# Kernel tuning notes

Hardware: AMD Instinct MI355X
Metric: run time of the kernel (lower is better)

The kernel has to match this reference:

```python
import jax, jax.numpy as jnp
import numpy as np

# model dims
V, D, DFF, H, NL = 8192, 1024, 4096, 16, 4
B, L, M = 2, 2048, 2048
S, R, W = 64, 1, 512          # chunk_size, chunk_rank, window_len
DH = D // H
NC = (L + M) // S             # total chunks over klen
NMC = M // S                  # memory chunks
NQC = L // S                  # query chunks in current block
NCV = NC * R                  # number of compressed chunk vectors
NT = L // W                   # window tiles

# static index/mask helpers (host-side numpy)
TILE_IDX = np.arange(NT)[:, None] * W + np.arange(2 * W)[None, :]          # (NT,2W) overlapping key tiles
DIAG_IDX = np.arange(W)[:, None] + 1 + np.arange(W)[None, :]               # (W,W): query q attends tile keys q+1..q+W
CIDX = np.arange(2 * W)[None, :] - np.arange(W)[:, None] - 1               # inverse map tile col -> band col
CVALID = (CIDX >= 0) & (CIDX < W)
_dist = (NMC + np.arange(NQC))[:, None] - np.arange(NC)[None, :]           # chunk distance (query chunk - key chunk)
PIDX = np.clip((NC - 1 - _dist)[:, :, None] * R + np.arange(R)[None, None, :], 0, NCV - 1).reshape(NQC, NCV)
CMASK = np.repeat(np.triu(np.ones((NQC, NC), dtype=bool), k=NMC), R, axis=1)  # mask key chunks >= own chunk


def layer_norm(x, g, b, eps=1e-5):
    mu = jnp.mean(x, -1, keepdims=True)
    var = jnp.mean((x - mu) ** 2, -1, keepdims=True)
    return (x - mu) * jax.lax.rsqrt(var + eps) * g + b


def sin_pos_emb(pos_seq, d):
    inv = jnp.asarray(1.0 / (10000.0 ** (np.arange(0, d, 2) / float(d))), jnp.float32)
    ang = pos_seq[:, None] * inv[None, :]
    return jnp.concatenate([jnp.sin(ang), jnp.cos(ang)], axis=-1)


def ls_attention(h, cache, Wq, Wk, Wv, Wo, w_dc, b_dc, Wr, Wrc, brc, rw, rr, gd, bd, gw, bw, pos_win, key_pe):
    # h: (B,L,D), cache: (B,M,D)
    def compress(seq):  # dynamic low-rank chunk compression
        n_ch = seq.shape[1] // S
        sc = (seq @ w_dc + b_dc).reshape(B, n_ch, S, H, R)
        sc = jax.nn.softmax(sc, axis=2)                       # softmax over chunk positions
        v = seq.reshape(B, n_ch, S, H, DH)
        return jnp.einsum('bcshr,bcshd->bcrhd', sc, v).reshape(B, n_ch * R, D)

    comp = jnp.concatenate([compress(cache), compress(h)], axis=1)           # (B,NCV,D)
    kc = layer_norm(comp @ Wk, gd, bd).reshape(B, NCV, H, DH).transpose(0, 2, 1, 3)
    vc = layer_norm(comp @ Wv, gd, bd).reshape(B, NCV, H, DH).transpose(0, 2, 1, 3)

    hw = jnp.concatenate([cache[:, -W:], h], axis=1)                         # (B,W+L,D)
    kw = layer_norm(hw @ Wk, gw, bw).reshape(B, W + L, H, DH)
    vw = layer_norm(hw @ Wv, gw, bw).reshape(B, W + L, H, DH)

    q = (h @ Wq).reshape(B, L, H, DH).transpose(0, 2, 1, 3) / np.float32(np.sqrt(DH))
    qw = q + rw[None, :, None, :]   # content bias
    qr = q + rr[None, :, None, :]   # position bias

    # ---- sliding-window attention (band width W, via overlapping tiles) ----
    kt = kw[:, TILE_IDX]            # (B,NT,2W,H,DH)
    vt = vw[:, TILE_IDX]
    ts = jnp.einsum('bhtqd,btkhd->bhtqk', qw.reshape(B, H, NT, W, DH), kt)   # (B,H,NT,W,2W)
    band = jnp.take_along_axis(ts, jnp.asarray(DIAG_IDX)[None, None, None], axis=-1)  # (B,H,NT,W,W)
    Pw = (pos_win @ Wr).reshape(W, H, DH)
    win_scores = band.reshape(B, H, L, W) + jnp.einsum('bhld,whd->bhlw', qr, Pw)

    # ---- compressed chunk attention with chunk-level relative positions ----
    cs = jnp.einsum('bhld,bhcd->bhlc', qw, kc)                               # (B,H,L,NCV)
    Pc = (key_pe @ Wrc + brc).reshape(NCV, H, DH)
    raw = jnp.einsum('bhld,phd->bhlp', qr, Pc)
    aligned = jnp.take_along_axis(raw.reshape(B, H, NQC, S, NCV), jnp.asarray(PIDX)[None, None, :, None, :], axis=-1)
    ch = cs.reshape(B, H, NQC, S, NCV) + aligned
    ch = jnp.where(jnp.asarray(CMASK)[None, None, :, None, :], -1e30, ch).reshape(B, H, L, NCV)

    # joint softmax over [window keys | chunk summaries] (DualLN makes scales compatible)
    probs = jax.nn.softmax(jnp.concatenate([win_scores, ch], axis=-1), axis=-1)
    pw_, pc_ = probs[..., :W], probs[..., W:]

    gath = jnp.take_along_axis(pw_.reshape(B, H, NT, W, W), jnp.asarray(np.clip(CIDX, 0, W - 1))[None, None, None], axis=-1)
    tileP = jnp.where(jnp.asarray(CVALID)[None, None, None], gath, 0.0)      # (B,H,NT,W,2W)
    out_w = jnp.einsum('bhtqk,btkhd->bhtqd', tileP, vt).reshape(B, H, L, DH)
    out_c = jnp.einsum('bhlc,bhcd->bhld', pc_, vc)
    return (out_w + out_c).transpose(0, 2, 1, 3).reshape(B, L, D) @ Wo


def setup_inputs() -> dict:
    key = jax.random.key(0)
    ks = jax.random.split(key, 20)
    n = lambda i, shape, s=0.02: jax.random.normal(ks[i], shape, jnp.float32) * s
    z = lambda shape: jnp.zeros(shape, jnp.float32)
    return {
        'x': jax.random.randint(ks[0], (B, L), 0, V, dtype=jnp.int32),
        'cache': n(1, (NL, B, M, D), 0.1),
        'emb': n(2, (V, D), float(D) ** -0.5),
        'out_bias': z((V,)),
        'Wq': n(3, (NL, D, D)), 'Wk': n(4, (NL, D, D)), 'Wv': n(5, (NL, D, D)), 'Wo': n(6, (NL, D, D)),
        'w_dc': n(7, (NL, D, H * R)), 'b_dc': z((NL, H * R)),
        'Wr': n(8, (NL, D, D)), 'Wrc': n(9, (NL, D, D)), 'brc': z((NL, D)),
        'rw': n(10, (NL, H, DH)), 'rr': n(11, (NL, H, DH)),
        'g1': 1.0 + n(12, (NL, D)), 'b1': z((NL, D)),
        'g2': 1.0 + n(13, (NL, D)), 'b2': z((NL, D)),
        'gd': 1.0 + n(14, (NL, D)), 'bd': z((NL, D)),
        'gw': 1.0 + n(15, (NL, D)), 'bw': z((NL, D)),
        'wf1': n(16, (NL, D, DFF)), 'bf1': z((NL, DFF)),
        'wf2': n(17, (NL, DFF, D)), 'bf2': z((NL, D)),
    }


def reference(x, cache, emb, out_bias, Wq, Wk, Wv, Wo, w_dc, b_dc, Wr, Wrc, brc, rw, rr,
              g1, b1, g2, b2, gd, bd, gw, bw, wf1, bf1, wf2, bf2):
    h = emb[x] * np.float32(np.sqrt(D))
    pos_win = sin_pos_emb(jnp.arange(W - 1, -1, -1, dtype=jnp.float32), D)
    key_pe = sin_pos_emb(jnp.arange(NCV - 1, -1, -1, dtype=jnp.float32), D)
    for l in range(NL):  # post-LN (pre_ln=False)
        a = ls_attention(h, cache[l], Wq[l], Wk[l], Wv[l], Wo[l], w_dc[l], b_dc[l], Wr[l], Wrc[l],
                         brc[l], rw[l], rr[l], gd[l], bd[l], gw[l], bw[l], pos_win, key_pe)
        h = layer_norm(h + a, g1[l], b1[l])
        ff = jax.nn.gelu(h @ wf1[l] + bf1[l], approximate=False) @ wf2[l] + bf2[l]
        h = layer_norm(h + ff, g2[l], b2[l])
    logits = h @ emb.T + out_bias   # tied output embedding
    return jax.nn.log_softmax(logits, axis=-1)
```

## Files before the change

kernel.cpp:

```cpp
#include <hip/hip_runtime.h>
#include <math.h>

constexpr int Bq   = 2;
constexpr int Lq   = 2048;
constexpr int Mq   = 2048;
constexpr int Dq   = 1024;
constexpr int DFFq = 4096;
constexpr int Hq   = 16;
constexpr int DHq  = 64;
constexpr int Vq   = 8192;
constexpr int NLq  = 4;
constexpr int Wwin = 512;
constexpr int NCVq = 64;
constexpr int HWLEN = Wwin + Lq;

constexpr size_t OFF_H    = 0;
constexpr size_t OFF_A    = OFF_H    + (size_t)Bq*Lq*Dq;
constexpr size_t OFF_ATT  = OFF_A    + (size_t)Bq*Lq*Dq;
constexpr size_t OFF_Q    = OFF_ATT  + (size_t)Bq*Lq*Dq;
constexpr size_t OFF_HW   = OFF_Q    + (size_t)Bq*Lq*Dq;
constexpr size_t OFF_KW   = OFF_HW   + (size_t)Bq*HWLEN*Dq;
constexpr size_t OFF_VW   = OFF_KW   + (size_t)Bq*HWLEN*Dq;
constexpr size_t OFF_FF   = OFF_VW   + (size_t)Bq*HWLEN*Dq;
constexpr size_t OFF_COMP = OFF_FF   + (size_t)Bq*Lq*DFFq;
constexpr size_t OFF_KC   = OFF_COMP + (size_t)Bq*NCVq*Dq;
constexpr size_t OFF_VC   = OFF_KC   + (size_t)Bq*NCVq*Dq;
constexpr size_t OFF_SCC  = OFF_VC   + (size_t)Bq*NCVq*Dq;
constexpr size_t OFF_SCH  = OFF_SCC  + (size_t)Bq*Mq*16;
constexpr size_t OFF_PWIN = OFF_SCH  + (size_t)Bq*Lq*16;
constexpr size_t OFF_KPE  = OFF_PWIN + (size_t)Wwin*Dq;
constexpr size_t OFF_PW   = OFF_KPE  + (size_t)NCVq*Dq;
constexpr size_t OFF_PC   = OFF_PW   + (size_t)Wwin*Dq;
constexpr size_t WS_FLOATS= OFF_PC   + (size_t)NCVq*Dq;

__global__ __launch_bounds__(256) void embed_kernel(const int* __restrict__ x,
                                                    const float* __restrict__ emb,
                                                    float* __restrict__ h) {
  int i = blockIdx.x * 256 + threadIdx.x;
  int tok = i >> 10;
  int d = i & 1023;
  h[i] = emb[(size_t)x[tok] * Dq + d] * 32.0f;
}

__global__ __launch_bounds__(256) void posemb_kernel(float* __restrict__ pwin,
                                                     float* __restrict__ kpe) {
  int i = blockIdx.x * 256 + threadIdx.x;
  int row = i >> 10, col = i & 1023;
  int ii = col & 511;
  bool is_cos = col >= 512;
  float invf = (float)exp(-((double)(2 * ii) / 1024.0) * log(10000.0));
  float* dst; float pos;
  if (row < Wwin) { dst = pwin + (size_t)row * Dq + col; pos = (float)(Wwin - 1 - row); }
  else { dst = kpe + (size_t)(row - Wwin) * Dq + col; pos = (float)(NCVq - 1 - (row - Wwin)); }
  float ang = pos * invf;
  *dst = is_cos ? cosf(ang) : sinf(ang);
}

template<int BT, int EPI>
__global__ __launch_bounds__(256) void gemm_kernel(const float* __restrict__ A,
                                                   const float* __restrict__ Bm,
                                                   const float* __restrict__ bias,
                                                   float* __restrict__ C,
                                                   int M, int N, int K) {
  __shared__ float As[16][64];
  __shared__ float Bs[16][64];
  const int tid = threadIdx.x;
  const int tx = tid & 15;
  const int ty = tid >> 4;
  const int m0 = blockIdx.y * 64;
  const int n0 = blockIdx.x * 64;
  const int ar = tid >> 2;
  const int ak = (tid & 3) << 2;
  float acc[4][4] = {};
  for (int k0 = 0; k0 < K; k0 += 16) {
    float4 av = *(const float4*)(A + (size_t)(m0 + ar) * K + (k0 + ak));
    As[ak + 0][ar] = av.x; As[ak + 1][ar] = av.y;
    As[ak + 2][ar] = av.z; As[ak + 3][ar] = av.w;
    if (BT == 0) {
      const int bk = tid >> 4;
      const int bc = (tid & 15) << 2;
      float4 bv = make_float4(0.f, 0.f, 0.f, 0.f);
      if (n0 + bc < N) bv = *(const float4*)(Bm + (size_t)(k0 + bk) * N + (n0 + bc));
      Bs[bk][bc + 0] = bv.x; Bs[bk][bc + 1] = bv.y;
      Bs[bk][bc + 2] = bv.z; Bs[bk][bc + 3] = bv.w;
    } else {
      const int c = tid >> 2;
      const int kk = (tid & 3) << 2;
      float4 bv = make_float4(0.f, 0.f, 0.f, 0.f);
      if (n0 + c < N) bv = *(const float4*)(Bm + (size_t)(n0 + c) * K + (k0 + kk));
      Bs[kk + 0][c] = bv.x; Bs[kk + 1][c] = bv.y;
      Bs[kk + 2][c] = bv.z; Bs[kk + 3][c] = bv.w;
    }
    __syncthreads();
#pragma unroll
    for (int k = 0; k < 16; ++k) {
      float4 a4 = *(const float4*)&As[k][ty << 2];
      float4 b4 = *(const float4*)&Bs[k][tx << 2];
      float aa[4] = {a4.x, a4.y, a4.z, a4.w};
      float bb[4] = {b4.x, b4.y, b4.z, b4.w};
#pragma unroll
      for (int i = 0; i < 4; ++i)
#pragma unroll
        for (int j = 0; j < 4; ++j) acc[i][j] += aa[i] * bb[j];
    }
    __syncthreads();
  }
  const int cbase = n0 + (tx << 2);
  if (cbase < N) {
#pragma unroll
    for (int i = 0; i < 4; ++i) {
      const int r = m0 + (ty << 2) + i;
      float4 o;
      float* op = &o.x;
#pragma unroll
      for (int j = 0; j < 4; ++j) {
        float v = acc[i][j];
        if (EPI >= 1) v += bias[cbase + j];
        if (EPI == 2) v = 0.5f * v * (1.0f + erff(v * 0.70710678118654752f));
        op[j] = v;
      }
      *(float4*)(C + (size_t)r * N + cbase) = o;
    }
  }
}

__global__ __launch_bounds__(256) void ln_kernel(const float* __restrict__ x,
                                                 const float* __restrict__ res,
                                                 const float* __restrict__ g,
                                                 const float* __restrict__ b,
                                                 float* __restrict__ out) {
  __shared__ float sm[4];
  const int row = blockIdx.x;
  const int t = threadIdx.x;
  const float* xp = x + (size_t)row * Dq;
  float v[4];
#pragma unroll
  for (int i = 0; i < 4; ++i) v[i] = xp[t + 256 * i];
  if (res) {
    const float* rp = res + (size_t)row * Dq;
#pragma unroll
    for (int i = 0; i < 4; ++i) v[i] += rp[t + 256 * i];
  }
  float s = v[0] + v[1] + v[2] + v[3];
#pragma unroll
  for (int off = 32; off > 0; off >>= 1) s += __shfl_down(s, off);
  if ((t & 63) == 0) sm[t >> 6] = s;
  __syncthreads();
  const float mu = (sm[0] + sm[1] + sm[2] + sm[3]) * (1.0f / Dq);
  __syncthreads();
  float s2 = 0.f;
#pragma unroll
  for (int i = 0; i < 4; ++i) { float d = v[i] - mu; s2 += d * d; }
#pragma unroll
  for (int off = 32; off > 0; off >>= 1) s2 += __shfl_down(s2, off);
  if ((t & 63) == 0) sm[t >> 6] = s2;
  __syncthreads();
  const float var = (sm[0] + sm[1] + sm[2] + sm[3]) * (1.0f / Dq);
  const float rstd = rsqrtf(var + 1e-5f);
  float* op = out + (size_t)row * Dq;
#pragma unroll
  for (int i = 0; i < 4; ++i) {
    int c = t + 256 * i;
    op[c] = (v[i] - mu) * rstd * g[c] + b[c];
  }
}

__global__ __launch_bounds__(64) void compress_kernel(const float* __restrict__ scc,
                                                      const float* __restrict__ sch,
                                                      const float* __restrict__ cache_l,
                                                      const float* __restrict__ h,
                                                      float* __restrict__ comp) {
  const int bi = blockIdx.x;
  const int head = bi & 15;
  const int c = (bi >> 4) & 63;
  const int b = bi >> 10;
  const bool from_cache = c < 32;
  const int cc = from_cache ? c : c - 32;
  const float* logits = (from_cache ? scc : sch) + (size_t)(b * 2048 + cc * 64) * 16 + head;
  const float* seq = (from_cache ? cache_l : h) + (size_t)(b * 2048 + cc * 64) * Dq + head * 64;
  __shared__ float wsm[64];
  const int t = threadIdx.x;
  wsm[t] = logits[(size_t)t * 16];
  __syncthreads();
  float mx = -1e30f;
#pragma unroll 8
  for (int s = 0; s < 64; ++s) mx = fmaxf(mx, wsm[s]);
  float sum = 0.f;
#pragma unroll 8
  for (int s = 0; s < 64; ++s) sum += expf(wsm[s] - mx);
  float myw = expf(wsm[t] - mx) / sum;
  __syncthreads();
  wsm[t] = myw;
  __syncthreads();
  float acc = 0.f;
#pragma unroll 4
  for (int s = 0; s < 64; ++s) acc += wsm[s] * seq[(size_t)s * Dq + t];
  comp[(size_t)(b * 64 + c) * Dq + head * 64 + t] = acc;
}

__global__ __launch_bounds__(256) void hwbuild_kernel(const float* __restrict__ cache_l,
                                                      const float* __restrict__ h,
                                                      float* __restrict__ hw) {
  int i = blockIdx.x * 256 + threadIdx.x;
  const int D4 = Dq / 4;
  int d4 = i % D4;
  int r = (i / D4) % HWLEN;
  int b = i / (HWLEN * D4);
  const float4* src;
  if (r < Wwin) src = (const float4*)(cache_l + (size_t)(b * Mq + (Mq - Wwin) + r) * Dq) + d4;
  else          src = (const float4*)(h + (size_t)(b * Lq + (r - Wwin)) * Dq) + d4;
  ((float4*)hw)[i] = *src;
}

__global__ __launch_bounds__(256) void attn_kernel(const float* __restrict__ q,
                                                   const float* __restrict__ kw,
                                                   const float* __restrict__ vw,
                                                   const float* __restrict__ kc,
                                                   const float* __restrict__ vc,
                                                   const float* __restrict__ Pw,
                                                   const float* __restrict__ Pc,
                                                   const float* __restrict__ rw,
                                                   const float* __restrict__ rr,
                                                   float* __restrict__ att) {
  __shared__ float qws[32][64];
  __shared__ float qrs[32][64];
  __shared__ float sc[32][580];
  __shared__ float ksf[64 * 64];
  const int blk = blockIdx.x;
  const int qblk = blk & 63;
  const int hh = (blk >> 6) & 15;
  const int b = blk >> 10;
  const int qbase = qblk * 32;
  const int qc = qblk >> 1;
  const int t = threadIdx.x;
  const int hoff = hh * 64;

#pragma unroll
  for (int i = 0; i < 8; ++i) {
    int e = t + 256 * i;
    int qi = e >> 6, d = e & 63;
    float qv = q[(size_t)(b * Lq + qbase + qi) * Dq + hoff + d] * 0.125f;
    qws[qi][d] = qv + rw[hoff + d];
    qrs[qi][d] = qv + rr[hoff + d];
  }
  __syncthreads();

  const int eq = t >> 6;
  const int ed = t & 63;

  for (int cb = 0; cb < 8; ++cb) {
#pragma unroll
    for (int i = 0; i < 16; ++i) {
      int e = t + 256 * i;
      int jj = e >> 6, d = e & 63;
      ksf[jj * 64 + (d ^ ((jj & 7) << 2))] = Pw[(size_t)(cb * 64 + jj) * Dq + hoff + d];
    }
    __syncthreads();
#pragma unroll
    for (int rs = 0; rs < 8; ++rs) {
      int qi = eq + 4 * rs;
      int jj = ed;
      float dot = 0.f;
#pragma unroll
      for (int d0 = 0; d0 < 64; d0 += 4) {
        float4 qv = *(const float4*)&qrs[qi][d0];
        float4 kv = *(const float4*)&ksf[jj * 64 + (d0 ^ ((jj & 7) << 2))];
        dot += qv.x * kv.x + qv.y * kv.y + qv.z * kv.z + qv.w * kv.w;
      }
      sc[qi][cb * 64 + jj] = dot;
    }
    __syncthreads();
  }

  for (int ci = 0; ci < 9; ++ci) {
    const int khw0 = qbase + 1 + ci * 64;
#pragma unroll
    for (int i = 0; i < 16; ++i) {
      int e = t + 256 * i;
      int kk = e >> 6, d = e & 63;
      int khw = khw0 + kk; if (khw > HWLEN - 1) khw = HWLEN - 1;
      ksf[kk * 64 + (d ^ ((kk & 7) << 2))] = kw[(size_t)(b * HWLEN + khw) * Dq + hoff + d];
    }
    __syncthreads();
#pragma unroll
    for (int rs = 0; rs < 8; ++rs) {
      int qi = eq + 4 * rs;
      int kk = ed;
      int j = ci * 64 + kk - qi;
      if (j >= 0 && j < 512) {
        float dot = 0.f;
#pragma unroll
        for (int d0 = 0; d0 < 64; d0 += 4) {
          float4 qv = *(const float4*)&qws[qi][d0];
          float4 kv = *(const float4*)&ksf[kk * 64 + (d0 ^ ((kk & 7) << 2))];
          dot += qv.x * kv.x + qv.y * kv.y + qv.z * kv.z + qv.w * kv.w;
        }
        sc[qi][j] += dot;
      }
    }
    __syncthreads();
  }

#pragma unroll
  for (int i = 0; i < 16; ++i) {
    int e = t + 256 * i;
    int cc = e >> 6, d = e & 63;
    ksf[cc * 64 + (d ^ ((cc & 7) << 2))] = kc[(size_t)(b * 64 + cc) * Dq + hoff + d];
  }
  __syncthreads();
#pragma unroll
  for (int rs = 0; rs < 8; ++rs) {
    int qi = eq + 4 * rs;
    int cc = ed;
    float dot = 0.f;
#pragma unroll
    for (int d0 = 0; d0 < 64; d0 += 4) {
      float4 qv = *(const float4*)&qws[qi][d0];
      float4 kv = *(const float4*)&ksf[cc * 64 + (d0 ^ ((cc & 7) << 2))];
      dot += qv.x * kv.x + qv.y * kv.y + qv.z * kv.z + qv.w * kv.w;
    }
    sc[qi][512 + cc] = dot;
  }
  __syncthreads();
#pragma unroll
  for (int i = 0; i < 16; ++i) {
    int e = t + 256 * i;
    int cc = e >> 6, d = e & 63;
    int pidx = 31 - qc + cc;
    pidx = pidx < 0 ? 0 : (pidx > 63 ? 63 : pidx);
    ksf[cc * 64 + (d ^ ((cc & 7) << 2))] = Pc[(size_t)pidx * Dq + hoff + d];
  }
  __syncthreads();
#pragma unroll
  for (int rs = 0; rs < 8; ++rs) {
    int qi = eq + 4 * rs;
    int cc = ed;
    float dot = 0.f;
#pragma unroll
    for (int d0 = 0; d0 < 64; d0 += 4) {
      float4 qv = *(const float4*)&qrs[qi][d0];
      float4 kv = *(const float4*)&ksf[cc * 64 + (d0 ^ ((cc & 7) << 2))];
      dot += qv.x * kv.x + qv.y * kv.y + qv.z * kv.z + qv.w * kv.w;
    }
    float vvv = sc[qi][512 + cc] + dot;
    sc[qi][512 + cc] = (cc >= qc + 32) ? -1e30f : vvv;
  }
  __syncthreads();

  {
    const int row = t >> 3;
    const int sub = t & 7;
    float m = -1e30f;
    for (int k = 0; k < 72; ++k) m = fmaxf(m, sc[row][sub + 8 * k]);
#pragma unroll
    for (int off = 1; off < 8; off <<= 1) m = fmaxf(m, __shfl_xor(m, off, 8));
    float ssum = 0.f;
    for (int k = 0; k < 72; ++k) ssum += expf(sc[row][sub + 8 * k] - m);
#pragma unroll
    for (int off = 1; off < 8; off <<= 1) ssum += __shfl_xor(ssum, off, 8);
    const float inv = 1.0f / ssum;
    for (int k = 0; k < 72; ++k) {
      int idx = sub + 8 * k;
      sc[row][idx] = expf(sc[row][idx] - m) * inv;
    }
  }
  __syncthreads();

  float acc[8] = {};
  const size_t vwbase = (size_t)b * HWLEN * Dq + hoff + ed;
  for (int j = 0; j < 512; ++j) {
#pragma unroll
    for (int rs = 0; rs < 8; ++rs) {
      int qi = eq + 4 * rs;
      acc[rs] += sc[qi][j] * vw[vwbase + (size_t)(qbase + qi + 1 + j) * Dq];
    }
  }
  const size_t vcbase = (size_t)b * 64 * Dq + hoff + ed;
  for (int cc = 0; cc < 64; ++cc) {
#pragma unroll
    for (int rs = 0; rs < 8; ++rs) {
      int qi = eq + 4 * rs;
      acc[rs] += sc[qi][512 + cc] * vc[vcbase + (size_t)cc * Dq];
    }
  }
#pragma unroll
  for (int rs = 0; rs < 8; ++rs) {
    int qi = eq + 4 * rs;
    att[(size_t)(b * Lq + qbase + qi) * Dq + hoff + ed] = acc[rs];
  }
}

__global__ __launch_bounds__(256) void logsoftmax_kernel(float* __restrict__ out) {
  __shared__ float sm[4];
  const int row = blockIdx.x;
  float* p = out + (size_t)row * Vq;
  const int t = threadIdx.x;
  float v[32];
  float m = -1e30f;
#pragma unroll
  for (int i = 0; i < 32; ++i) { v[i] = p[t + 256 * i]; m = fmaxf(m, v[i]); }
#pragma unroll
  for (int off = 32; off > 0; off >>= 1) m = fmaxf(m, __shfl_xor(m, off));
  if ((t & 63) == 0) sm[t >> 6] = m;
  __syncthreads();
  m = fmaxf(fmaxf(sm[0], sm[1]), fmaxf(sm[2], sm[3]));
  __syncthreads();
  float s = 0.f;
#pragma unroll
  for (int i = 0; i < 32; ++i) s += expf(v[i] - m);
#pragma unroll
  for (int off = 32; off > 0; off >>= 1) s += __shfl_down(s, off);
  if ((t & 63) == 0) sm[t >> 6] = s;
  __syncthreads();
  const float lse = m + logf(sm[0] + sm[1] + sm[2] + sm[3]);
#pragma unroll
  for (int i = 0; i < 32; ++i) p[t + 256 * i] = v[i] - lse;
}

extern "C" void kernel_launch(void* const* d_in, const int* in_sizes, int n_in,
                              void* d_out, int out_size, void* d_ws, size_t ws_size,
                              hipStream_t stream) {
  if (ws_size < WS_FLOATS * sizeof(float)) return;

  const int*   x        = (const int*)d_in[0];
  const float* cache    = (const float*)d_in[1];
  const float* emb      = (const float*)d_in[2];
  const float* out_bias = (const float*)d_in[3];
  const float* Wqw      = (const float*)d_in[4];
  const float* Wkw      = (const float*)d_in[5];
  const float* Wvw      = (const float*)d_in[6];
  const float* Wow      = (const float*)d_in[7];
  const float* w_dc     = (const float*)d_in[8];
  const float* b_dc     = (const float*)d_in[9];
  const float* Wr       = (const float*)d_in[10];
  const float* Wrc      = (const float*)d_in[11];
  const float* brc      = (const float*)d_in[12];
  const float* rw       = (const float*)d_in[13];
  const float* rr       = (const float*)d_in[14];
  const float* g1       = (const float*)d_in[15];
  const float* b1       = (const float*)d_in[16];
  const float* g2       = (const float*)d_in[17];
  const float* b2       = (const float*)d_in[18];
  const float* gd       = (const float*)d_in[19];
  const float* bd       = (const float*)d_in[20];
  const float* gw       = (const float*)d_in[21];
  const float* bw       = (const float*)d_in[22];
  const float* wf1      = (const float*)d_in[23];
  const float* bf1      = (const float*)d_in[24];
  const float* wf2      = (const float*)d_in[25];
  const float* bf2      = (const float*)d_in[26];

  float* ws   = (float*)d_ws;
  float* hbuf = ws + OFF_H;
  float* abuf = ws + OFF_A;
  float* attb = ws + OFF_ATT;
  float* qb   = ws + OFF_Q;
  float* hwb  = ws + OFF_HW;
  float* kwb  = ws + OFF_KW;
  float* vwb  = ws + OFF_VW;
  float* ffb  = ws + OFF_FF;
  float* comp = ws + OFF_COMP;
  float* kcb  = ws + OFF_KC;
  float* vcb  = ws + OFF_VC;
  float* scc  = ws + OFF_SCC;
  float* sch  = ws + OFF_SCH;
  float* pwin = ws + OFF_PWIN;
  float* kpe  = ws + OFF_KPE;
  float* Pwb  = ws + OFF_PW;
  float* Pcb  = ws + OFF_PC;
  float* outp = (float*)d_out;

  embed_kernel<<<(Bq * Lq * Dq) / 256, 256, 0, stream>>>(x, emb, hbuf);
  posemb_kernel<<<((Wwin + NCVq) * Dq) / 256, 256, 0, stream>>>(pwin, kpe);

  for (int l = 0; l < NLq; ++l) {
    const float* cache_l = cache + (size_t)l * Bq * Mq * Dq;
    const float* Wq_l  = Wqw + (size_t)l * Dq * Dq;
    const float* Wk_l  = Wkw + (size_t)l * Dq * Dq;
    const float* Wv_l  = Wvw + (size_t)l * Dq * Dq;
    const float* Wo_l  = Wow + (size_t)l * Dq * Dq;
    const float* wdc_l = w_dc + (size_t)l * Dq * 16;
    const float* bdc_l = b_dc + (size_t)l * 16;
    const float* Wr_l  = Wr  + (size_t)l * Dq * Dq;
    const float* Wrc_l = Wrc + (size_t)l * Dq * Dq;
    const float* brc_l = brc + (size_t)l * Dq;
    const float* rw_l  = rw  + (size_t)l * Hq * DHq;
    const float* rr_l  = rr  + (size_t)l * Hq * DHq;
    const float* g1_l  = g1 + (size_t)l * Dq;  const float* b1_l = b1 + (size_t)l * Dq;
    const float* g2_l  = g2 + (size_t)l * Dq;  const float* b2_l = b2 + (size_t)l * Dq;
    const float* gd_l  = gd + (size_t)l * Dq;  const float* bd_l = bd + (size_t)l * Dq;
    const float* gw_l  = gw + (size_t)l * Dq;  const float* bw_l = bw + (size_t)l * Dq;
    const float* wf1_l = wf1 + (size_t)l * Dq * DFFq;
    const float* bf1_l = bf1 + (size_t)l * DFFq;
    const float* wf2_l = wf2 + (size_t)l * DFFq * Dq;
    const float* bf2_l = bf2 + (size_t)l * Dq;

    gemm_kernel<0, 1><<<dim3(1, 64), 256, 0, stream>>>(cache_l, wdc_l, bdc_l, scc, Bq * Mq, 16, Dq);
    gemm_kernel<0, 1><<<dim3(1, 64), 256, 0, stream>>>(hbuf, wdc_l, bdc_l, sch, Bq * Lq, 16, Dq);
    compress_kernel<<<Bq * 64 * Hq, 64, 0, stream>>>(scc, sch, cache_l, hbuf, comp);
    gemm_kernel<0, 0><<<dim3(16, 2), 256, 0, stream>>>(comp, Wk_l, nullptr, kcb, Bq * NCVq, Dq, Dq);
    ln_kernel<<<Bq * NCVq, 256, 0, stream>>>(kcb, nullptr, gd_l, bd_l, kcb);
    gemm_kernel<0, 0><<<dim3(16, 2), 256, 0, stream>>>(comp, Wv_l, nullptr, vcb, Bq * NCVq, Dq, Dq);
    ln_kernel<<<Bq * NCVq, 256, 0, stream>>>(vcb, nullptr, gd_l, bd_l, vcb);
    hwbuild_kernel<<<(Bq * HWLEN * (Dq / 4)) / 256, 256, 0, stream>>>(cache_l, hbuf, hwb);
    gemm_kernel<0, 0><<<dim3(16, 80), 256, 0, stream>>>(hwb, Wk_l, nullptr, kwb, Bq * HWLEN, Dq, Dq);
    ln_kernel<<<Bq * HWLEN, 256, 0, stream>>>(kwb, nullptr, gw_l, bw_l, kwb);
    gemm_kernel<0, 0><<<dim3(16, 80), 256, 0, stream>>>(hwb, Wv_l, nullptr, vwb, Bq * HWLEN, Dq, Dq);
    ln_kernel<<<Bq * HWLEN, 256, 0, stream>>>(vwb, nullptr, gw_l, bw_l, vwb);
    gemm_kernel<0, 0><<<dim3(16, 64), 256, 0, stream>>>(hbuf, Wq_l, nullptr, qb, Bq * Lq, Dq, Dq);
    gemm_kernel<0, 0><<<dim3(16, 8), 256, 0, stream>>>(pwin, Wr_l, nullptr, Pwb, Wwin, Dq, Dq);
    gemm_kernel<0, 1><<<dim3(16, 1), 256, 0, stream>>>(kpe, Wrc_l, brc_l, Pcb, NCVq, Dq, Dq);
    attn_kernel<<<Bq * Hq * 64, 256, 0, stream>>>(qb, kwb, vwb, kcb, vcb, Pwb, Pcb, rw_l, rr_l, attb);
    gemm_kernel<0, 0><<<dim3(16, 64), 256, 0, stream>>>(attb, Wo_l, nullptr, abuf, Bq * Lq, Dq, Dq);
    ln_kernel<<<Bq * Lq, 256, 0, stream>>>(hbuf, abuf, g1_l, b1_l, hbuf);
    gemm_kernel<0, 2><<<dim3(64, 64), 256, 0, stream>>>(hbuf, wf1_l, bf1_l, ffb, Bq * Lq, DFFq, Dq);
    gemm_kernel<0, 1><<<dim3(16, 64), 256, 0, stream>>>(ffb, wf2_l, bf2_l, abuf, Bq * Lq, Dq, DFFq);
    ln_kernel<<<Bq * Lq, 256, 0, stream>>>(hbuf, abuf, g2_l, b2_l, hbuf);
  }

  gemm_kernel<1, 1><<<dim3(Vq / 64, (Bq * Lq) / 64), 256, 0, stream>>>(hbuf, emb, out_bias, outp,
                                                                       Bq * Lq, Vq, Dq);
  logsoftmax_kernel<<<Bq * Lq, 256, 0, stream>>>(outp);
}
```

Measured before the change: 16.99 ms.

## Move large GEMMs to bf16 MFMA kernels and restructure attention for 1024 threads

Replaces the fp32 SIMT GEMMs for the projection, FFN and output-logit matmuls with a bf16 MFMA GEMM using global_load_lds staging. Weights are transposed and converted to bf16 every call, and activations are converted before each GEMM. The attention kernel is reworked to use 1024 threads, and its PV stage now stages V tiles through LDS instead of reading global memory per element. The conversion kernels add traffic, and bf16 inputs lower precision compared with fp32.

```diff
diff --git a/kernel.cpp b/kernel.cpp
--- a/kernel.cpp
+++ b/kernel.cpp
@@ -7,31 +7,56 @@
 constexpr int Dq   = 1024;
 constexpr int DFFq = 4096;
 constexpr int Hq   = 16;
-constexpr int DHq  = 64;
 constexpr int Vq   = 8192;
 constexpr int NLq  = 4;
 constexpr int Wwin = 512;
 constexpr int NCVq = 64;
 constexpr int HWLEN = Wwin + Lq;
 
-constexpr size_t OFF_H    = 0;
-constexpr size_t OFF_A    = OFF_H    + (size_t)Bq*Lq*Dq;
-constexpr size_t OFF_ATT  = OFF_A    + (size_t)Bq*Lq*Dq;
-constexpr size_t OFF_Q    = OFF_ATT  + (size_t)Bq*Lq*Dq;
-constexpr size_t OFF_HW   = OFF_Q    + (size_t)Bq*Lq*Dq;
-constexpr size_t OFF_KW   = OFF_HW   + (size_t)Bq*HWLEN*Dq;
-constexpr size_t OFF_VW   = OFF_KW   + (size_t)Bq*HWLEN*Dq;
-constexpr size_t OFF_FF   = OFF_VW   + (size_t)Bq*HWLEN*Dq;
-constexpr size_t OFF_COMP = OFF_FF   + (size_t)Bq*Lq*DFFq;
-constexpr size_t OFF_KC   = OFF_COMP + (size_t)Bq*NCVq*Dq;
-constexpr size_t OFF_VC   = OFF_KC   + (size_t)Bq*NCVq*Dq;
-constexpr size_t OFF_SCC  = OFF_VC   + (size_t)Bq*NCVq*Dq;
-constexpr size_t OFF_SCH  = OFF_SCC  + (size_t)Bq*Mq*16;
-constexpr size_t OFF_PWIN = OFF_SCH  + (size_t)Bq*Lq*16;
-constexpr size_t OFF_KPE  = OFF_PWIN + (size_t)Wwin*Dq;
-constexpr size_t OFF_PW   = OFF_KPE  + (size_t)NCVq*Dq;
-constexpr size_t OFF_PC   = OFF_PW   + (size_t)Wwin*Dq;
-constexpr size_t WS_FLOATS= OFF_PC   + (size_t)NCVq*Dq;
+constexpr size_t F_H    = 0;
+constexpr size_t F_ATT  = F_H    + 4194304;
+constexpr size_t F_Q    = F_ATT  + 4194304;
+constexpr size_t F_HW   = F_Q    + 4194304;
+constexpr size_t F_KW   = F_HW   + 5242880;
+constexpr size_t F_VW   = F_KW   + 5242880;
+constexpr size_t F_COMP = F_VW   + 5242880;
+constexpr size_t F_KC   = F_COMP + 131072;
+constexpr size_t F_VC   = F_KC   + 131072;
+constexpr size_t F_SCC  = F_VC   + 131072;
+constexpr size_t F_SCH  = F_SCC  + 65536;
+constexpr size_t F_PWIN = F_SCH  + 65536;
+constexpr size_t F_KPE  = F_PWIN + 524288;
+constexpr size_t F_PWB  = F_KPE  + 65536;
+constexpr size_t F_PCB  = F_PWB  + 524288;
+constexpr size_t F_BF   = F_PCB  + 65536;
+constexpr size_t U_WT     = 0;
+constexpr size_t U_WQT    = U_WT + 0;
+constexpr size_t U_WKT    = U_WT + 1048576;
+constexpr size_t U_WVT    = U_WT + 2097152;
+constexpr size_t U_WOT    = U_WT + 3145728;
+constexpr size_t U_WRT    = U_WT + 4194304;
+constexpr size_t U_WF1T   = U_WT + 5242880;
+constexpr size_t U_WF2T   = U_WT + 9437184;
+constexpr size_t U_HBF    = 13631488;
+constexpr size_t U_HWBF   = U_HBF + 4194304;
+constexpr size_t U_FFBF   = U_HWBF + 5242880;
+constexpr size_t U_COMPBF = U_FFBF + 16777216;
+constexpr size_t U_PWINBF = U_COMPBF + 131072;
+constexpr size_t U_END    = U_PWINBF + 524288;
+constexpr size_t WS_FLOATS = F_BF + (U_END + 1) / 2;
+
+__device__ __forceinline__ unsigned short f2bf(float f) {
+  union { float f; unsigned u; } c; c.f = f;
+  unsigned u = c.u + 0x7fffu + ((c.u >> 16) & 1u);
+  return (unsigned short)(u >> 16);
+}
+
+typedef __attribute__((ext_vector_type(8))) short short8v;
+typedef __attribute__((ext_vector_type(4))) float f32x4v;
+
+#define GLOAD16(gp, lp)                                                              \
+  __builtin_amdgcn_global_load_lds((const __attribute__((address_space(1))) void*)(gp), \
+                                   (__attribute__((address_space(3))) void*)(lp), 16, 0, 0)
 
 __global__ __launch_bounds__(256) void embed_kernel(const int* __restrict__ x,
                                                     const float* __restrict__ emb,
@@ -54,6 +79,108 @@
   else { dst = kpe + (size_t)(row - Wwin) * Dq + col; pos = (float)(NCVq - 1 - (row - Wwin)); }
   float ang = pos * invf;
   *dst = is_cos ? cosf(ang) : sinf(ang);
+}
+
+__global__ __launch_bounds__(256) void cvt_bf16_kernel(const float* __restrict__ in,
+                                                       unsigned short* __restrict__ out) {
+  int i = blockIdx.x * 256 + threadIdx.x;
+  float4 v = ((const float4*)in)[i];
+  ushort4 o;
+  o.x = f2bf(v.x); o.y = f2bf(v.y); o.z = f2bf(v.z); o.w = f2bf(v.w);
+  ((ushort4*)out)[i] = o;
+}
+
+__global__ __launch_bounds__(256) void tcvt_kernel(const float* __restrict__ W,
+                                                   unsigned short* __restrict__ Wt,
+                                                   int K, int N) {
+  __shared__ float tile[64][65];
+  const int n0 = blockIdx.x * 64, k0 = blockIdx.y * 64;
+  const int tr = threadIdx.x >> 6;
+  const int tc = threadIdx.x & 63;
+#pragma unroll
+  for (int i = 0; i < 16; ++i) {
+    int r = i * 4 + tr;
+    tile[r][tc] = W[(size_t)(k0 + r) * N + n0 + tc];
+  }
+  __syncthreads();
+#pragma unroll
+  for (int i = 0; i < 16; ++i) {
+    int r = i * 4 + tr;
+    Wt[(size_t)(n0 + r) * K + k0 + tc] = f2bf(tile[tc][r]);
+  }
+}
+
+template<int EPI>
+__global__ __launch_bounds__(256) void gemm_bf16_kernel(const unsigned short* __restrict__ A,
+                                                        const unsigned short* __restrict__ Bt,
+                                                        const float* __restrict__ bias,
+                                                        void* __restrict__ Cout,
+                                                        int M, int N, int K) {
+  __shared__ unsigned short ldsA[8 * 512];
+  __shared__ unsigned short ldsB[8 * 512];
+  const int t = threadIdx.x;
+  const int wave = t >> 6, lane = t & 63;
+  const int m0 = blockIdx.y * 128, n0 = blockIdx.x * 128;
+  const int fr = lane & 15, fg = lane >> 4;
+  const unsigned short* Ab = A + (size_t)(m0 + fr) * K + fg * 8;
+  const unsigned short* Bb = Bt + (size_t)(n0 + fr) * K + fg * 8;
+  const int wr = wave >> 1, wc = wave & 1;
+  f32x4v acc[4][4];
+#pragma unroll
+  for (int i = 0; i < 4; ++i)
+#pragma unroll
+    for (int j = 0; j < 4; ++j) acc[i][j] = (f32x4v){0.f, 0.f, 0.f, 0.f};
+
+  for (int k0 = 0; k0 < K; k0 += 32) {
+    __syncthreads();
+    if (wave < 2) {
+#pragma unroll
+      for (int i = 0; i < 4; ++i) {
+        int sb = wave * 4 + i;
+        GLOAD16(Ab + (size_t)(sb * 16) * K + k0, &ldsA[sb * 512]);
+      }
+    } else {
+#pragma unroll
+      for (int i = 0; i < 4; ++i) {
+        int sb = (wave - 2) * 4 + i;
+        GLOAD16(Bb + (size_t)(sb * 16) * K + k0, &ldsB[sb * 512]);
+      }
+    }
+    __syncthreads();
+    short8v af[4], bf[4];
+#pragma unroll
+    for (int i = 0; i < 4; ++i) {
+      af[i] = *(const short8v*)&ldsA[(wr * 4 + i) * 512 + lane * 8];
+      bf[i] = *(const short8v*)&ldsB[(wc * 4 + i) * 512 + lane * 8];
+    }
+#pragma unroll
+    for (int i = 0; i < 4; ++i)
+#pragma unroll
+      for (int j = 0; j < 4; ++j)
+        acc[i][j] = __builtin_amdgcn_mfma_f32_16x16x32_bf16(af[i], bf[j], acc[i][j], 0, 0, 0);
+  }
+
+  const int orow0 = m0 + wr * 64 + (lane >> 4) * 4;
+  const int ocol0 = n0 + wc * 64 + (lane & 15);
+#pragma unroll
+  for (int i = 0; i < 4; ++i) {
+#pragma unroll
+    for (int j = 0; j < 4; ++j) {
+      const int col = ocol0 + j * 16;
+      float bv = (EPI >= 1) ? bias[col] : 0.f;
+#pragma unroll
+      for (int r = 0; r < 4; ++r) {
+        const int row = orow0 + i * 16 + r;
+        float v = acc[i][j][r] + bv;
+        if (EPI == 2) {
+          v = 0.5f * v * (1.0f + erff(v * 0.70710678118654752f));
+          ((unsigned short*)Cout)[(size_t)row * N + col] = f2bf(v);
+        } else {
+          ((float*)Cout)[(size_t)row * N + col] = v;
+        }
+      }
+    }
+  }
 }
 
 template<int BT, int EPI>
@@ -212,20 +339,20 @@
   ((float4*)hw)[i] = *src;
 }
 
-__global__ __launch_bounds__(256) void attn_kernel(const float* __restrict__ q,
-                                                   const float* __restrict__ kw,
-                                                   const float* __restrict__ vw,
-                                                   const float* __restrict__ kc,
-                                                   const float* __restrict__ vc,
-                                                   const float* __restrict__ Pw,
-                                                   const float* __restrict__ Pc,
-                                                   const float* __restrict__ rw,
-                                                   const float* __restrict__ rr,
-                                                   float* __restrict__ att) {
+__global__ __launch_bounds__(1024) void attn_kernel(const float* __restrict__ q,
+                                                    const float* __restrict__ kw,
+                                                    const float* __restrict__ vw,
+                                                    const float* __restrict__ kc,
+                                                    const float* __restrict__ vc,
+                                                    const float* __restrict__ Pw,
+                                                    const float* __restrict__ Pc,
+                                                    const float* __restrict__ rw,
+                                                    const float* __restrict__ rr,
+                                                    float* __restrict__ att) {
   __shared__ float qws[32][64];
   __shared__ float qrs[32][64];
   __shared__ float sc[32][580];
-  __shared__ float ksf[64 * 64];
+  __shared__ float ksf[4096];
   const int blk = blockIdx.x;
   const int qblk = blk & 63;
   const int hh = (blk >> 6) & 15;
@@ -236,8 +363,8 @@
   const int hoff = hh * 64;
 
 #pragma unroll
-  for (int i = 0; i < 8; ++i) {
-    int e = t + 256 * i;
+  for (int i = 0; i < 2; ++i) {
+    int e = t + 1024 * i;
     int qi = e >> 6, d = e & 63;
     float qv = q[(size_t)(b * Lq + qbase + qi) * Dq + hoff + d] * 0.125f;
     qws[qi][d] = qv + rw[hoff + d];
@@ -250,24 +377,23 @@
 
   for (int cb = 0; cb < 8; ++cb) {
 #pragma unroll
-    for (int i = 0; i < 16; ++i) {
-      int e = t + 256 * i;
+    for (int i = 0; i < 4; ++i) {
+      int e = t + 1024 * i;
       int jj = e >> 6, d = e & 63;
       ksf[jj * 64 + (d ^ ((jj & 7) << 2))] = Pw[(size_t)(cb * 64 + jj) * Dq + hoff + d];
     }
     __syncthreads();
 #pragma unroll
-    for (int rs = 0; rs < 8; ++rs) {
-      int qi = eq + 4 * rs;
-      int jj = ed;
+    for (int rs = 0; rs < 2; ++rs) {
+      int qi = eq + 16 * rs;
       float dot = 0.f;
 #pragma unroll
       for (int d0 = 0; d0 < 64; d0 += 4) {
         float4 qv = *(const float4*)&qrs[qi][d0];
-        float4 kv = *(const float4*)&ksf[jj * 64 + (d0 ^ ((jj & 7) << 2))];
+        float4 kv = *(const float4*)&ksf[ed * 64 + (d0 ^ ((ed & 7) << 2))];
         dot += qv.x * kv.x + qv.y * kv.y + qv.z * kv.z + qv.w * kv.w;
       }
-      sc[qi][cb * 64 + jj] = dot;
+      sc[qi][cb * 64 + ed] = dot;
     }
     __syncthreads();
   }
@@ -275,24 +401,23 @@
   for (int ci = 0; ci < 9; ++ci) {
     const int khw0 = qbase + 1 + ci * 64;
 #pragma unroll
-    for (int i = 0; i < 16; ++i) {
-      int e = t + 256 * i;
+    for (int i = 0; i < 4; ++i) {
+      int e = t + 1024 * i;
       int kk = e >> 6, d = e & 63;
       int khw = khw0 + kk; if (khw > HWLEN - 1) khw = HWLEN - 1;
       ksf[kk * 64 + (d ^ ((kk & 7) << 2))] = kw[(size_t)(b * HWLEN + khw) * Dq + hoff + d];
     }
     __syncthreads();
 #pragma unroll
-    for (int rs = 0; rs < 8; ++rs) {
-      int qi = eq + 4 * rs;
-      int kk = ed;
-      int j = ci * 64 + kk - qi;
+    for (int rs = 0; rs < 2; ++rs) {
+      int qi = eq + 16 * rs;
+      int j = ci * 64 + ed - qi;
       if (j >= 0 && j < 512) {
         float dot = 0.f;
 #pragma unroll
         for (int d0 = 0; d0 < 64; d0 += 4) {
           float4 qv = *(const float4*)&qws[qi][d0];
-          float4 kv = *(const float4*)&ksf[kk * 64 + (d0 ^ ((kk & 7) << 2))];
+          float4 kv = *(const float4*)&ksf[ed * 64 + (d0 ^ ((ed & 7) << 2))];
           dot += qv.x * kv.x + qv.y * kv.y + qv.z * kv.z + qv.w * kv.w;
         }
         sc[qi][j] += dot;
@@ -301,93 +426,121 @@
     __syncthreads();
   }
 
-#pragma unroll
-  for (int i = 0; i < 16; ++i) {
-    int e = t + 256 * i;
-    int cc = e >> 6, d = e & 63;
-    ksf[cc * 64 + (d ^ ((cc & 7) << 2))] = kc[(size_t)(b * 64 + cc) * Dq + hoff + d];
-  }
-  __syncthreads();
-#pragma unroll
-  for (int rs = 0; rs < 8; ++rs) {
-    int qi = eq + 4 * rs;
-    int cc = ed;
-    float dot = 0.f;
-#pragma unroll
-    for (int d0 = 0; d0 < 64; d0 += 4) {
-      float4 qv = *(const float4*)&qws[qi][d0];
-      float4 kv = *(const float4*)&ksf[cc * 64 + (d0 ^ ((cc & 7) << 2))];
-      dot += qv.x * kv.x + qv.y * kv.y + qv.z * kv.z + qv.w * kv.w;
-    }
-    sc[qi][512 + cc] = dot;
-  }
-  __syncthreads();
-#pragma unroll
-  for (int i = 0; i < 16; ++i) {
-    int e = t + 256 * i;
-    int cc = e >> 6, d = e & 63;
-    int pidx = 31 - qc + cc;
-    pidx = pidx < 0 ? 0 : (pidx > 63 ? 63 : pidx);
-    ksf[cc * 64 + (d ^ ((cc & 7) << 2))] = Pc[(size_t)pidx * Dq + hoff + d];
-  }
-  __syncthreads();
-#pragma unroll
-  for (int rs = 0; rs < 8; ++rs) {
-    int qi = eq + 4 * rs;
-    int cc = ed;
-    float dot = 0.f;
-#pragma unroll
-    for (int d0 = 0; d0 < 64; d0 += 4) {
-      float4 qv = *(const float4*)&qrs[qi][d0];
-      float4 kv = *(const float4*)&ksf[cc * 64 + (d0 ^ ((cc & 7) << 2))];
-      dot += qv.x * kv.x + qv.y * kv.y + qv.z * kv.z + qv.w * kv.w;
-    }
-    float vvv = sc[qi][512 + cc] + dot;
-    sc[qi][512 + cc] = (cc >= qc + 32) ? -1e30f : vvv;
-  }
-  __syncthreads();
-
   {
-    const int row = t >> 3;
-    const int sub = t & 7;
+#pragma unroll
+    for (int i = 0; i < 4; ++i) {
+      int e = t + 1024 * i;
+      int cc = e >> 6, d = e & 63;
+      ksf[cc * 64 + (d ^ ((cc & 7) << 2))] = kc[(size_t)(b * 64 + cc) * Dq + hoff + d];
+    }
+    __syncthreads();
+#pragma unroll
+    for (int rs = 0; rs < 2; ++rs) {
+      int qi = eq + 16 * rs;
+      float dot = 0.f;
+#pragma unroll
+      for (int d0 = 0; d0 < 64; d0 += 4) {
+        float4 qv = *(const float4*)&qws[qi][d0];
+        float4 kv = *(const float4*)&ksf[ed * 64 + (d0 ^ ((ed & 7) << 2))];
+        dot += qv.x * kv.x + qv.y * kv.y + qv.z * kv.z + qv.w * kv.w;
+      }
+      sc[qi][512 + ed] = dot;
+    }
+    __syncthreads();
+  }
+  {
+#pragma unroll
+    for (int i = 0; i < 4; ++i) {
+      int e = t + 1024 * i;
+      int cc = e >> 6, d = e & 63;
+      int pidx = 31 - qc + cc;
+      pidx = pidx < 0 ? 0 : (pidx > 63 ? 63 : pidx);
+      ksf[cc * 64 + (d ^ ((cc & 7) << 2))] = Pc[(size_t)pidx * Dq + hoff + d];
+    }
+    __syncthreads();
+#pragma unroll
+    for (int rs = 0; rs < 2; ++rs) {
+      int qi = eq + 16 * rs;
+      float dot = 0.f;
+#pragma unroll
+      for (int d0 = 0; d0 < 64; d0 += 4) {
+        float4 qv = *(const float4*)&qrs[qi][d0];
+        float4 kv = *(const float4*)&ksf[ed * 64 + (d0 ^ ((ed & 7) << 2))];
+        dot += qv.x * kv.x + qv.y * kv.y + qv.z * kv.z + qv.w * kv.w;
+      }
+      float vvv = sc[qi][512 + ed] + dot;
+      sc[qi][512 + ed] = (ed >= qc + 32) ? -1e30f : vvv;
+    }
+    __syncthreads();
+  }
+
+  {
+    const int row = t >> 5;
+    const int sub = t & 31;
     float m = -1e30f;
-    for (int k = 0; k < 72; ++k) m = fmaxf(m, sc[row][sub + 8 * k]);
-#pragma unroll
-    for (int off = 1; off < 8; off <<= 1) m = fmaxf(m, __shfl_xor(m, off, 8));
+#pragma unroll
+    for (int k = 0; k < 18; ++k) m = fmaxf(m, sc[row][sub + 32 * k]);
+#pragma unroll
+    for (int off = 1; off < 32; off <<= 1) m = fmaxf(m, __shfl_xor(m, off, 32));
     float ssum = 0.f;
-    for (int k = 0; k < 72; ++k) ssum += expf(sc[row][sub + 8 * k] - m);
-#pragma unroll
-    for (int off = 1; off < 8; off <<= 1) ssum += __shfl_xor(ssum, off, 8);
+#pragma unroll
+    for (int k = 0; k < 18; ++k) {
+      float p = expf(sc[row][sub + 32 * k] - m);
+      sc[row][sub + 32 * k] = p;
+      ssum += p;
+    }
+#pragma unroll
+    for (int off = 1; off < 32; off <<= 1) ssum += __shfl_xor(ssum, off, 32);
     const float inv = 1.0f / ssum;
-    for (int k = 0; k < 72; ++k) {
-      int idx = sub + 8 * k;
-      sc[row][idx] = expf(sc[row][idx] - m) * inv;
-    }
-  }
-  __syncthreads();
-
-  float acc[8] = {};
-  const size_t vwbase = (size_t)b * HWLEN * Dq + hoff + ed;
-  for (int j = 0; j < 512; ++j) {
-#pragma unroll
-    for (int rs = 0; rs < 8; ++rs) {
-      int qi = eq + 4 * rs;
-      acc[rs] += sc[qi][j] * vw[vwbase + (size_t)(qbase + qi + 1 + j) * Dq];
-    }
-  }
-  const size_t vcbase = (size_t)b * 64 * Dq + hoff + ed;
-  for (int cc = 0; cc < 64; ++cc) {
-#pragma unroll
-    for (int rs = 0; rs < 8; ++rs) {
-      int qi = eq + 4 * rs;
-      acc[rs] += sc[qi][512 + cc] * vc[vcbase + (size_t)cc * Dq];
-    }
-  }
-#pragma unroll
-  for (int rs = 0; rs < 8; ++rs) {
-    int qi = eq + 4 * rs;
-    att[(size_t)(b * Lq + qbase + qi) * Dq + hoff + ed] = acc[rs];
-  }
+#pragma unroll
+    for (int k = 0; k < 18; ++k) sc[row][sub + 32 * k] *= inv;
+  }
+  __syncthreads();
+
+  float acc0 = 0.f, acc1 = 0.f;
+  for (int ci = 0; ci < 9; ++ci) {
+    const int khw0 = qbase + 1 + ci * 64;
+#pragma unroll
+    for (int i = 0; i < 4; ++i) {
+      int e = t + 1024 * i;
+      int kk = e >> 6, d = e & 63;
+      int khw = khw0 + kk; if (khw > HWLEN - 1) khw = HWLEN - 1;
+      ksf[kk * 64 + (d ^ ((kk & 7) << 2))] = vw[(size_t)(b * HWLEN + khw) * Dq + hoff + d];
+    }
+    __syncthreads();
+#pragma unroll
+    for (int rs = 0; rs < 2; ++rs) {
+      int qi = eq + 16 * rs;
+      int lo = qi - ci * 64; if (lo < 0) lo = 0;
+      int hi = 512 + qi - ci * 64; if (hi > 64) hi = 64;
+      float a = 0.f;
+      for (int kk = lo; kk < hi; ++kk) {
+        a += sc[qi][ci * 64 + kk - qi] * ksf[kk * 64 + (ed ^ ((kk & 7) << 2))];
+      }
+      if (rs == 0) acc0 += a; else acc1 += a;
+    }
+    __syncthreads();
+  }
+  {
+#pragma unroll
+    for (int i = 0; i < 4; ++i) {
+      int e = t + 1024 * i;
+      int cc = e >> 6, d = e & 63;
+      ksf[cc * 64 + (d ^ ((cc & 7) << 2))] = vc[(size_t)(b * 64 + cc) * Dq + hoff + d];
+    }
+    __syncthreads();
+#pragma unroll
+    for (int rs = 0; rs < 2; ++rs) {
+      int qi = eq + 16 * rs;
+      float a = 0.f;
+      for (int cc = 0; cc < 64; ++cc) {
+        a += sc[qi][512 + cc] * ksf[cc * 64 + (ed ^ ((cc & 7) << 2))];
+      }
+      if (rs == 0) acc0 += a; else acc1 += a;
+    }
+  }
+  att[(size_t)(b * Lq + qbase + eq) * Dq + hoff + ed] = acc0;
+  att[(size_t)(b * Lq + qbase + eq + 16) * Dq + hoff + ed] = acc1;
 }
 
 __global__ __launch_bounds__(256) void logsoftmax_kernel(float* __restrict__ out) {
@@ -451,27 +604,42 @@
   const float* bf2      = (const float*)d_in[26];
 
   float* ws   = (float*)d_ws;
-  float* hbuf = ws + OFF_H;
-  float* abuf = ws + OFF_A;
-  float* attb = ws + OFF_ATT;
-  float* qb   = ws + OFF_Q;
-  float* hwb  = ws + OFF_HW;
-  float* kwb  = ws + OFF_KW;
-  float* vwb  = ws + OFF_VW;
-  float* ffb  = ws + OFF_FF;
-  float* comp = ws + OFF_COMP;
-  float* kcb  = ws + OFF_KC;
-  float* vcb  = ws + OFF_VC;
-  float* scc  = ws + OFF_SCC;
-  float* sch  = ws + OFF_SCH;
-  float* pwin = ws + OFF_PWIN;
-  float* kpe  = ws + OFF_KPE;
-  float* Pwb  = ws + OFF_PW;
-  float* Pcb  = ws + OFF_PC;
+  float* hbuf = ws + F_H;
+  float* attb = ws + F_ATT;
+  float* abuf = ws + F_ATT;
+  float* qb   = ws + F_Q;
+  float* hwb  = ws + F_HW;
+  float* kwb  = ws + F_KW;
+  float* vwb  = ws + F_VW;
+  float* comp = ws + F_COMP;
+  float* kcb  = ws + F_KC;
+  float* vcb  = ws + F_VC;
+  float* scc  = ws + F_SCC;
+  float* sch  = ws + F_SCH;
+  float* pwin = ws + F_PWIN;
+  float* kpe  = ws + F_KPE;
+  float* Pwb  = ws + F_PWB;
+  float* Pcb  = ws + F_PCB;
+  unsigned short* bfb    = (unsigned short*)(ws + F_BF);
+  unsigned short* WqT    = bfb + U_WQT;
+  unsigned short* WkT    = bfb + U_WKT;
+  unsigned short* WvT    = bfb + U_WVT;
+  unsigned short* WoT    = bfb + U_WOT;
+  unsigned short* WrT    = bfb + U_WRT;
+  unsigned short* WF1T   = bfb + U_WF1T;
+  unsigned short* WF2T   = bfb + U_WF2T;
+  unsigned short* hbf    = bfb + U_HBF;
+  unsigned short* hwbf   = bfb + U_HWBF;
+  unsigned short* attbf  = bfb + U_HWBF;
+  unsigned short* ffbf   = bfb + U_FFBF;
+  unsigned short* embbf  = bfb + U_FFBF;
+  unsigned short* compbf = bfb + U_COMPBF;
+  unsigned short* pwinbf = bfb + U_PWINBF;
   float* outp = (float*)d_out;
 
   embed_kernel<<<(Bq * Lq * Dq) / 256, 256, 0, stream>>>(x, emb, hbuf);
   posemb_kernel<<<((Wwin + NCVq) * Dq) / 256, 256, 0, stream>>>(pwin, kpe);
+  cvt_bf16_kernel<<<(Wwin * Dq) / 1024, 256, 0, stream>>>(pwin, pwinbf);
 
   for (int l = 0; l < NLq; ++l) {
     const float* cache_l = cache + (size_t)l * Bq * Mq * Dq;
@@ -484,8 +652,8 @@
     const float* Wr_l  = Wr  + (size_t)l * Dq * Dq;
     const float* Wrc_l = Wrc + (size_t)l * Dq * Dq;
     const float* brc_l = brc + (size_t)l * Dq;
-    const float* rw_l  = rw  + (size_t)l * Hq * DHq;
-    const float* rr_l  = rr  + (size_t)l * Hq * DHq;
+    const float* rw_l  = rw  + (size_t)l * Hq * 64;
+    const float* rr_l  = rr  + (size_t)l * Hq * 64;
     const float* g1_l  = g1 + (size_t)l * Dq;  const float* b1_l = b1 + (size_t)l * Dq;
     const float* g2_l  = g2 + (size_t)l * Dq;  const float* b2_l = b2 + (size_t)l * Dq;
     const float* gd_l  = gd + (size_t)l * Dq;  const float* bd_l = bd + (size_t)l * Dq;
@@ -495,30 +663,45 @@
     const float* wf2_l = wf2 + (size_t)l * DFFq * Dq;
     const float* bf2_l = bf2 + (size_t)l * Dq;
 
+    tcvt_kernel<<<dim3(16, 16), 256, 0, stream>>>(Wq_l, WqT, Dq, Dq);
+    tcvt_kernel<<<dim3(16, 16), 256, 0, stream>>>(Wk_l, WkT, Dq, Dq);
+    tcvt_kernel<<<dim3(16, 16), 256, 0, stream>>>(Wv_l, WvT, Dq, Dq);
+    tcvt_kernel<<<dim3(16, 16), 256, 0, stream>>>(Wo_l, WoT, Dq, Dq);
+    tcvt_kernel<<<dim3(16, 16), 256, 0, stream>>>(Wr_l, WrT, Dq, Dq);
+    tcvt_kernel<<<dim3(64, 16), 256, 0, stream>>>(wf1_l, WF1T, Dq, DFFq);
+    tcvt_kernel<<<dim3(16, 64), 256, 0, stream>>>(wf2_l, WF2T, DFFq, Dq);
+
     gemm_kernel<0, 1><<<dim3(1, 64), 256, 0, stream>>>(cache_l, wdc_l, bdc_l, scc, Bq * Mq, 16, Dq);
     gemm_kernel<0, 1><<<dim3(1, 64), 256, 0, stream>>>(hbuf, wdc_l, bdc_l, sch, Bq * Lq, 16, Dq);
     compress_kernel<<<Bq * 64 * Hq, 64, 0, stream>>>(scc, sch, cache_l, hbuf, comp);
-    gemm_kernel<0, 0><<<dim3(16, 2), 256, 0, stream>>>(comp, Wk_l, nullptr, kcb, Bq * NCVq, Dq, Dq);
+    cvt_bf16_kernel<<<(Bq * NCVq * Dq) / 1024, 256, 0, stream>>>(comp, compbf);
+    gemm_bf16_kernel<0><<<dim3(8, 1), 256, 0, stream>>>(compbf, WkT, nullptr, kcb, Bq * NCVq, Dq, Dq);
     ln_kernel<<<Bq * NCVq, 256, 0, stream>>>(kcb, nullptr, gd_l, bd_l, kcb);
-    gemm_kernel<0, 0><<<dim3(16, 2), 256, 0, stream>>>(comp, Wv_l, nullptr, vcb, Bq * NCVq, Dq, Dq);
+    gemm_bf16_kernel<0><<<dim3(8, 1), 256, 0, stream>>>(compbf, WvT, nullptr, vcb, Bq * NCVq, Dq, Dq);
     ln_kernel<<<Bq * NCVq, 256, 0, stream>>>(vcb, nullptr, gd_l, bd_l, vcb);
     hwbuild_kernel<<<(Bq * HWLEN * (Dq / 4)) / 256, 256, 0, stream>>>(cache_l, hbuf, hwb);
-    gemm_kernel<0, 0><<<dim3(16, 80), 256, 0, stream>>>(hwb, Wk_l, nullptr, kwb, Bq * HWLEN, Dq, Dq);
+    cvt_bf16_kernel<<<(Bq * HWLEN * Dq) / 1024, 256, 0, stream>>>(hwb, hwbf);
+    gemm_bf16_kernel<0><<<dim3(8, 40), 256, 0, stream>>>(hwbf, WkT, nullptr, kwb, Bq * HWLEN, Dq, Dq);
     ln_kernel<<<Bq * HWLEN, 256, 0, stream>>>(kwb, nullptr, gw_l, bw_l, kwb);
-    gemm_kernel<0, 0><<<dim3(16, 80), 256, 0, stream>>>(hwb, Wv_l, nullptr, vwb, Bq * HWLEN, Dq, Dq);
+    gemm_bf16_kernel<0><<<dim3(8, 40), 256, 0, stream>>>(hwbf, WvT, nullptr, vwb, Bq * HWLEN, Dq, Dq);
     ln_kernel<<<Bq * HWLEN, 256, 0, stream>>>(vwb, nullptr, gw_l, bw_l, vwb);
-    gemm_kernel<0, 0><<<dim3(16, 64), 256, 0, stream>>>(hbuf, Wq_l, nullptr, qb, Bq * Lq, Dq, Dq);
-    gemm_kernel<0, 0><<<dim3(16, 8), 256, 0, stream>>>(pwin, Wr_l, nullptr, Pwb, Wwin, Dq, Dq);
+    cvt_bf16_kernel<<<(Bq * Lq * Dq) / 1024, 256, 0, stream>>>(hbuf, hbf);
+    gemm_bf16_kernel<0><<<dim3(8, 32), 256, 0, stream>>>(hbf, WqT, nullptr, qb, Bq * Lq, Dq, Dq);
+    gemm_bf16_kernel<0><<<dim3(8, 4), 256, 0, stream>>>(pwinbf, WrT, nullptr, Pwb, Wwin, Dq, Dq);
     gemm_kernel<0, 1><<<dim3(16, 1), 256, 0, stream>>>(kpe, Wrc_l, brc_l, Pcb, NCVq, Dq, Dq);
-    attn_kernel<<<Bq * Hq * 64, 256, 0, stream>>>(qb, kwb, vwb, kcb, vcb, Pwb, Pcb, rw_l, rr_l, attb);
-    gemm_kernel<0, 0><<<dim3(16, 64), 256, 0, stream>>>(attb, Wo_l, nullptr, abuf, Bq * Lq, Dq, Dq);
+    attn_kernel<<<Bq * Hq * 64, 1024, 0, stream>>>(qb, kwb, vwb, kcb, vcb, Pwb, Pcb, rw_l, rr_l, attb);
+    cvt_bf16_kernel<<<(Bq * Lq * Dq) / 1024, 256, 0, stream>>>(attb, attbf);
+    gemm_bf16_kernel<0><<<dim3(8, 32), 256, 0, stream>>>(attbf, WoT, nullptr, abuf, Bq * Lq, Dq, Dq);
     ln_kernel<<<Bq * Lq, 256, 0, stream>>>(hbuf, abuf, g1_l, b1_l, hbuf);
-    gemm_kernel<0, 2><<<dim3(64, 64), 256, 0, stream>>>(hbuf, wf1_l, bf1_l, ffb, Bq * Lq, DFFq, Dq);
-    gemm_kernel<0, 1><<<dim3(16, 64), 256, 0, stream>>>(ffb, wf2_l, bf2_l, abuf, Bq * Lq, Dq, DFFq);
+    cvt_bf16_kernel<<<(Bq * Lq * Dq) / 1024, 256, 0, stream>>>(hbuf, hbf);
+    gemm_bf16_kernel<2><<<dim3(32, 32), 256, 0, stream>>>(hbf, WF1T, bf1_l, ffbf, Bq * Lq, DFFq, Dq);
+    gemm_bf16_kernel<1><<<dim3(8, 32), 256, 0, stream>>>(ffbf, WF2T, bf2_l, abuf, Bq * Lq, Dq, DFFq);
     ln_kernel<<<Bq * Lq, 256, 0, stream>>>(hbuf, abuf, g2_l, b2_l, hbuf);
   }
 
-  gemm_kernel<1, 1><<<dim3(Vq / 64, (Bq * Lq) / 64), 256, 0, stream>>>(hbuf, emb, out_bias, outp,
-                                                                       Bq * Lq, Vq, Dq);
+  cvt_bf16_kernel<<<(Bq * Lq * Dq) / 1024, 256, 0, stream>>>(hbuf, hbf);
+  cvt_bf16_kernel<<<(Vq * Dq) / 1024, 256, 0, stream>>>(emb, embbf);
+  gemm_bf16_kernel<1><<<dim3(Vq / 128, (Bq * Lq) / 128), 256, 0, stream>>>(hbf, embbf, out_bias,
+                                                                           outp, Bq * Lq, Vq, Dq);
   logsoftmax_kernel<<<Bq * Lq, 256, 0, stream>>>(outp);
 }
```

Measured after the change: 24.25 ms. 1.43x slower.
